# Performance work log

Hardware: AMD Instinct MI355X
Metric: run time of the kernel (lower is better)

Reference implementation:

```python
import jax, jax.numpy as jnp
import numpy as np

DIM = 768
HEADS = 12
HEAD_DIM = DIM // HEADS          # 64
M = int(DIM * 0.5)               # 384 random features
HIDDEN = int(DIM * 4.0)          # 3072
SCALE = HEAD_DIM ** (-0.25)
EPSILON = 1e-8
LN_EPS = 1e-5


def _orf(key):
    # per-head block-orthogonal random features, scaled by sqrt(m)
    def one(k):
        a = jax.random.normal(k, (M, HEAD_DIM))
        q, _ = jnp.linalg.qr(a)          # (M, HEAD_DIM), orthonormal columns
        return q.T                        # (HEAD_DIM, M), orthonormal rows
    ks = jax.random.split(key, HEADS)
    return jax.vmap(one)(ks) * np.sqrt(M)  # (H, HEAD_DIM, M)


def setup_inputs() -> dict:
    key = jax.random.key(0)
    ks = jax.random.split(key, 8)
    s = 0.02
    return {
        "x": jax.random.normal(ks[0], (32, 1024, DIM), jnp.float32),
        "ln1_g": jnp.ones((DIM,), jnp.float32),
        "ln1_b": jnp.zeros((DIM,), jnp.float32),
        "qkv_w": jax.random.normal(ks[1], (DIM, 3 * DIM), jnp.float32) * s,
        "qkv_b": jnp.zeros((3 * DIM,), jnp.float32),
        "w_orf": _orf(ks[2]).astype(jnp.float32),
        "proj_w": jax.random.normal(ks[3], (DIM, DIM), jnp.float32) * s,
        "proj_b": jnp.zeros((DIM,), jnp.float32),
        "ln2_g": jnp.ones((DIM,), jnp.float32),
        "ln2_b": jnp.zeros((DIM,), jnp.float32),
        "fc1_w": jax.random.normal(ks[4], (DIM, HIDDEN), jnp.float32) * s,
        "fc1_b": jnp.zeros((HIDDEN,), jnp.float32),
        "fc2_w": jax.random.normal(ks[5], (HIDDEN, DIM), jnp.float32) * s,
        "fc2_b": jnp.zeros((DIM,), jnp.float32),
    }


def _layernorm(x, g, b):
    mu = jnp.mean(x, axis=-1, keepdims=True)
    var = jnp.mean(jnp.square(x - mu), axis=-1, keepdims=True)
    return (x - mu) * jax.lax.rsqrt(var + LN_EPS) * g + b


def _feature_map(x, w):
    # x: (B,H,N,C), w: (H,C,M) -> exp(x*scale @ w - ||x*scale||^2/2)/sqrt(M)
    xs = x * SCALE
    proj = jnp.einsum("bhnc,hcm->bhnm", xs, w)
    sq = 0.5 * jnp.sum(xs * xs, axis=-1, keepdims=True)
    return jnp.exp(proj - sq) / np.sqrt(M)


def _performer_attn(x, qkv_w, qkv_b, w_orf, proj_w, proj_b):
    B, N, _ = x.shape
    qkv = x @ qkv_w + qkv_b                       # (B,N,3*DIM)
    qkv = qkv.reshape(B, N, 3, HEADS, HEAD_DIM)
    qkv = jnp.transpose(qkv, (2, 0, 3, 1, 4))     # (3,B,H,N,C)
    q = _feature_map(qkv[0], w_orf)               # (B,H,N,M)
    k = _feature_map(qkv[1], w_orf)               # (B,H,N,M)
    v = qkv[2]                                    # (B,H,N,C)
    k_sum = jnp.sum(k, axis=2)                    # (B,H,M)
    D = jnp.einsum("bhnm,bhm->bhn", q, k_sum)[..., None] + EPSILON
    ktv = jnp.einsum("bhnm,bhnc->bhmc", k, v)     # (B,H,M,C)
    out = jnp.einsum("bhnm,bhmc->bhnc", q, ktv) / D
    out = jnp.transpose(out, (0, 2, 1, 3)).reshape(B, N, DIM)
    return out @ proj_w + proj_b


def reference(x, ln1_g, ln1_b, qkv_w, qkv_b, w_orf, proj_w, proj_b,
              ln2_g, ln2_b, fc1_w, fc1_b, fc2_w, fc2_b):
    h = x + _performer_attn(_layernorm(x, ln1_g, ln1_b),
                            qkv_w, qkv_b, w_orf, proj_w, proj_b)
    y = _layernorm(h, ln2_g, ln2_b)
    y = jax.nn.gelu(y @ fc1_w + fc1_b) @ fc2_w + fc2_b
    return h + y
```

## Files before the change

### kernel.cpp

```cpp
#include <hip/hip_runtime.h>
#include <hip/hip_bf16.h>

#define NTOK   32768
#define BATCH  32
#define SEQ    1024
#define DIMD   768
#define HEADS  12
#define HDIM   64
#define MFEAT  384
#define HIDDEN 3072
#define SCALE  0.35355339059327379f
#define HALF_SCALE2 0.0625f
#define EPSP   3.84e-6f
#define WSCL   64.0f
#define IWSCL  0.015625f

typedef __attribute__((ext_vector_type(8))) short bf16x8;
typedef __attribute__((ext_vector_type(4))) float f32x4;
typedef __attribute__((ext_vector_type(2))) long long llong2;

static __device__ __forceinline__ float bf2f(unsigned short u) {
    return __uint_as_float(((unsigned)u) << 16);
}
static __device__ __forceinline__ unsigned short f2bf(float f) {
    unsigned u = __float_as_uint(f);
    return (unsigned short)((u + 0x7FFFu + ((u >> 16) & 1u)) >> 16);
}
static __device__ __forceinline__ unsigned char f2e4m3(float f) {
    unsigned u = __float_as_uint(f);
    const unsigned char s = (unsigned char)((u >> 24) & 0x80);
    const float af = __uint_as_float(u & 0x7FFFFFFF);
    if (!(af < 464.0f)) return s | 0x7E;
    int e = (int)((u >> 23) & 0xFF) - 127;
    if (e < -6) e = -6;
    const float ulp = __uint_as_float((unsigned)((e - 3 + 127) << 23));
    const float q = rintf(af / ulp) * ulp;
    if (q == 0.0f) return s;
    const unsigned v = __float_as_uint(q);
    const int qe = (int)((v >> 23) & 0xFF) - 127;
    if (qe < -6) return s | (unsigned char)(q * 512.0f);
    return s | (unsigned char)(((qe + 7) << 3) | ((v >> 20) & 7));
}
static __device__ __forceinline__ unsigned char f2e4m3_hw(float v) {
    unsigned r = 0;
    asm("v_cvt_pk_fp8_f32 %0, %1, %1" : "+v"(r) : "v"(v));
    return (unsigned char)(r & 0xFF);
}
static __device__ __forceinline__ int kperm(int kl) {
    return ((kl & 31) >> 3) * 16 + ((kl >> 5) << 3) + (kl & 7);
}
static __device__ __forceinline__ float gelu_fast(float v) {
    const float c = 0.7978845608028654f;
    const float u = c * v * (1.0f + 0.044715f * v * v);
    return v / (1.0f + __expf(-2.0f * u));
}
static __device__ __forceinline__ void gload16(const void* g, void* l) {
    __builtin_amdgcn_global_load_lds(
        (const __attribute__((address_space(1))) void*)g,
        (__attribute__((address_space(3))) void*)l, 16, 0, 0);
}

template <int OT>
__global__ __launch_bounds__(256) void ln_vec(
    const float* __restrict__ x, const float* __restrict__ g,
    const float* __restrict__ bta, void* __restrict__ o) {
    const size_t row = blockIdx.x;
    const float* xr = x + row * DIMD;
    const int t = threadIdx.x;
    float4 v = make_float4(0.f, 0.f, 0.f, 0.f);
    if (t < 192) v = *(const float4*)(xr + t * 4);
    float s  = v.x + v.y + v.z + v.w;
    float sq = v.x * v.x + v.y * v.y + v.z * v.z + v.w * v.w;
    const int lane = t & 63, w = t >> 6;
    #pragma unroll
    for (int off = 32; off > 0; off >>= 1) {
        s  += __shfl_down(s, off, 64);
        sq += __shfl_down(sq, off, 64);
    }
    __shared__ float red[2][4];
    if (lane == 0) { red[0][w] = s; red[1][w] = sq; }
    __syncthreads();
    s  = red[0][0] + red[0][1] + red[0][2] + red[0][3];
    sq = red[1][0] + red[1][1] + red[1][2] + red[1][3];
    const float mu  = s * (1.0f / DIMD);
    const float var = sq * (1.0f / DIMD) - mu * mu;
    const float r = rsqrtf(var + 1e-5f);
    if (t < 192) {
        const float4 gv = *(const float4*)(g + t * 4);
        const float4 bv = *(const float4*)(bta + t * 4);
        const float o0 = (v.x - mu) * r * gv.x + bv.x;
        const float o1 = (v.y - mu) * r * gv.y + bv.y;
        const float o2 = (v.z - mu) * r * gv.z + bv.z;
        const float o3 = (v.w - mu) * r * gv.w + bv.w;
        if constexpr (OT == 1) {
            unsigned short* orow = (unsigned short*)o + row * DIMD + t * 4;
            *(ushort4*)orow = make_ushort4(f2bf(o0), f2bf(o1), f2bf(o2), f2bf(o3));
        } else {
            const int k = t * 4;
            const int kb = k & ~63, kl = k & 63;
            unsigned char* orow = (unsigned char*)o + row * DIMD + kb + kperm(kl);
            uchar4 p; p.x = f2e4m3(o0); p.y = f2e4m3(o1);
            p.z = f2e4m3(o2); p.w = f2e4m3(o3);
            *(uchar4*)orow = p;
        }
    }
}

__global__ __launch_bounds__(256) void wconv(
    const float* __restrict__ W, unsigned short* __restrict__ Wt, int K, int N) {
    __shared__ float tile[32][33];
    const int n0 = blockIdx.x << 5, k0 = blockIdx.y << 5;
    const int tn = threadIdx.x & 31, tg = threadIdx.x >> 5;
    #pragma unroll
    for (int i = 0; i < 4; ++i) {
        const int k = (tg << 2) + i;
        tile[k][tn] = W[(size_t)(k0 + k) * N + n0 + tn];
    }
    __syncthreads();
    #pragma unroll
    for (int i = 0; i < 4; ++i) {
        const int n = (tg << 2) + i;
        Wt[(size_t)(n0 + n) * K + k0 + tn] = f2bf(tile[tn][n]);
    }
}

__global__ __launch_bounds__(256) void wconv_f8(
    const float* __restrict__ W, unsigned char* __restrict__ Wt, int K, int N) {
    __shared__ float tile[32][33];
    const int n0 = blockIdx.x << 5, k0 = blockIdx.y << 5;
    const int tn = threadIdx.x & 31, tg = threadIdx.x >> 5;
    #pragma unroll
    for (int i = 0; i < 4; ++i) {
        const int k = (tg << 2) + i;
        tile[k][tn] = W[(size_t)(k0 + k) * N + n0 + tn];
    }
    __syncthreads();
    #pragma unroll
    for (int i = 0; i < 4; ++i) {
        const int n = (tg << 2) + i;
        const int k = k0 + tn;
        const int kb = k & ~63, kl = k & 63;
        Wt[(size_t)(n0 + n) * K + kb + kperm(kl)] = f2e4m3(WSCL * tile[tn][n]);
    }
}

__global__ __launch_bounds__(256) void wprep(
    const float* __restrict__ worf, unsigned short* __restrict__ worf_ts) {
    __shared__ float tile[32][33];
    const int m0 = blockIdx.x << 5, c0 = blockIdx.y << 5, h = blockIdx.z;
    const int tn = threadIdx.x & 31, tg = threadIdx.x >> 5;
    #pragma unroll
    for (int i = 0; i < 4; ++i) {
        const int c = (tg << 2) + i;
        tile[c][tn] = worf[(size_t)(h * HDIM + c0 + c) * MFEAT + m0 + tn];
    }
    __syncthreads();
    #pragma unroll
    for (int i = 0; i < 4; ++i) {
        const int m = (tg << 2) + i;
        worf_ts[(size_t)(h * MFEAT + m0 + m) * HDIM + c0 + tn] =
            f2bf(SCALE * tile[tn][m]);
    }
}

template <int ACT, bool RES, bool OBF16>
__global__ __launch_bounds__(256, 2) void gemm_mfma(
    const unsigned short* __restrict__ A, const unsigned short* __restrict__ Wt,
    const float* __restrict__ bias, const float* __restrict__ resid,
    void* __restrict__ Craw, int K, int N) {
    __shared__ unsigned short As[3][128 * 32];
    __shared__ unsigned short Bs[3][128 * 32];
    const int t = threadIdx.x;
    const int w = t >> 6, l = t & 63;
    const int ncol = gridDim.x;
    const int lin = blockIdx.y * ncol + blockIdx.x;
    const int cpx = (ncol * gridDim.y) >> 3;
    const int wg = (lin & 7) * cpx + (lin >> 3);
    const int row0 = (wg / ncol) << 7, col0 = (wg % ncol) << 7;
    const int wr = (w >> 1) << 6, wc = (w & 1) << 6;

    const int sc = (((l & 3) ^ ((l >> 3) & 3)) << 3);
    const unsigned short* ag0 = A  + (size_t)(row0 + w * 32 + (l >> 2)) * K + sc;
    const unsigned short* ag1 = ag0 + (size_t)16 * K;
    const unsigned short* bg0 = Wt + (size_t)(col0 + w * 32 + (l >> 2)) * K + sc;
    const unsigned short* bg1 = bg0 + (size_t)16 * K;

    f32x4 acc[4][4] = {};
    const int NT = K >> 5;

    auto stage = [&](int bi, int s) {
        const size_t ko = (size_t)s << 5;
        gload16(ag0 + ko, &As[bi][w * 1024]);
        gload16(ag1 + ko, &As[bi][w * 1024 + 512]);
        gload16(bg0 + ko, &Bs[bi][w * 1024]);
        gload16(bg1 + ko, &Bs[bi][w * 1024 + 512]);
    };

    stage(0, 0);
    stage(1, 1);
    const int lr = l & 15, lg = l >> 4;
    const int lkx = (lg << 3) ^ ((((lr >> 1) & 3)) << 3);
    int cur = 0;
    for (int s = 0; s < NT; ++s) {
        if (s + 1 < NT) asm volatile("s_waitcnt vmcnt(4)" ::: "memory");
        else            asm volatile("s_waitcnt vmcnt(0)" ::: "memory");
        __builtin_amdgcn_s_barrier();
        __builtin_amdgcn_sched_barrier(0);
        if (s + 2 < NT) {
            int sb = cur + 2; if (sb >= 3) sb -= 3;
            stage(sb, s + 2);
        }
        const unsigned short* ab = &As[cur][0];
        const unsigned short* bb = &Bs[cur][0];
        bf16x8 af[4], bfr[4];
        #pragma unroll
        for (int f = 0; f < 4; ++f) {
            af[f]  = *(const bf16x8*)(ab + (wr + f * 16 + lr) * 32 + lkx);
            bfr[f] = *(const bf16x8*)(bb + (wc + f * 16 + lr) * 32 + lkx);
        }
        #pragma unroll
        for (int fi = 0; fi < 4; ++fi)
            #pragma unroll
            for (int fj = 0; fj < 4; ++fj)
                acc[fi][fj] = __builtin_amdgcn_mfma_f32_16x16x32_bf16(
                    af[fi], bfr[fj], acc[fi][fj], 0, 0, 0);
        cur = (cur + 1 == 3) ? 0 : cur + 1;
    }

    float bv[4];
    #pragma unroll
    for (int fj = 0; fj < 4; ++fj) bv[fj] = bias[col0 + wc + fj * 16 + lr];
    #pragma unroll
    for (int fi = 0; fi < 4; ++fi) {
        #pragma unroll
        for (int r = 0; r < 4; ++r) {
            const int row = row0 + wr + fi * 16 + lg * 4 + r;
            const size_t base = (size_t)row * N + col0 + wc + lr;
            #pragma unroll
            for (int fj = 0; fj < 4; ++fj) {
                float v = acc[fi][fj][r] + bv[fj];
                if constexpr (RES) v += resid[base + fj * 16];
                if constexpr (ACT == 1) v = gelu_fast(v);
                if constexpr (OBF16) ((unsigned short*)Craw)[base + fj * 16] = f2bf(v);
                else                 ((float*)Craw)[base + fj * 16] = v;
            }
        }
    }
}

template <int ACT, bool RES, int OT>
__global__ __launch_bounds__(256, 2) void gemm_fp8(
    const unsigned char* __restrict__ A, const unsigned char* __restrict__ Wt,
    const float* __restrict__ bias, const float* __restrict__ resid,
    void* __restrict__ Craw, int K, int N) {
    __shared__ unsigned char As[3][8192];
    __shared__ unsigned char Bs[3][8192];
    const int t = threadIdx.x;
    const int w = t >> 6, l = t & 63;
    const int ncol = gridDim.x;
    const int lin = blockIdx.y * ncol + blockIdx.x;
    const int cpx = (ncol * gridDim.y) >> 3;
    const int wg = (lin & 7) * cpx + (lin >> 3);
    const int row0 = (wg / ncol) << 7, col0 = (wg % ncol) << 7;
    const int wr = (w >> 1) << 6, wc = (w & 1) << 6;

    const int sc = (((l & 3) ^ ((l >> 3) & 3)) << 4);
    const unsigned char* ag0 = A  + (size_t)(row0 + w * 32 + (l >> 2)) * K + sc;
    const unsigned char* ag1 = ag0 + (size_t)16 * K;
    const unsigned char* bg0 = Wt + (size_t)(col0 + w * 32 + (l >> 2)) * K + sc;
    const unsigned char* bg1 = bg0 + (size_t)16 * K;

    f32x4 acc[4][4] = {};
    const int NT = K >> 6;

    auto stage = [&](int bi, int s) {
        const size_t ko = (size_t)s << 6;
        gload16(ag0 + ko, &As[bi][w * 2048]);
        gload16(ag1 + ko, &As[bi][w * 2048 + 1024]);
        gload16(bg0 + ko, &Bs[bi][w * 2048]);
        gload16(bg1 + ko, &Bs[bi][w * 2048 + 1024]);
    };

    stage(0, 0);
    stage(1, 1);
    const int lr = l & 15, lg = l >> 4;
    const int xoff = ((lg ^ ((lr >> 1) & 3)) << 4);
    int cur = 0;
    for (int s = 0; s < NT; ++s) {
        if (s + 1 < NT) asm volatile("s_waitcnt vmcnt(4)" ::: "memory");
        else            asm volatile("s_waitcnt vmcnt(0)" ::: "memory");
        __builtin_amdgcn_s_barrier();
        __builtin_amdgcn_sched_barrier(0);
        if (s + 2 < NT) {
            int sb = cur + 2; if (sb >= 3) sb -= 3;
            stage(sb, s + 2);
        }
        const unsigned char* ab = &As[cur][0];
        const unsigned char* bb = &Bs[cur][0];
        llong2 av[4], bvv[4];
        #pragma unroll
        for (int f = 0; f < 4; ++f) {
            av[f]  = *(const llong2*)(ab + ((wr + f * 16 + lr) << 6) + xoff);
            bvv[f] = *(const llong2*)(bb + ((wc + f * 16 + lr) << 6) + xoff);
        }
        #pragma unroll
        for (int ks = 0; ks < 2; ++ks)
            #pragma unroll
            for (int fi = 0; fi < 4; ++fi)
                #pragma unroll
                for (int fj = 0; fj < 4; ++fj)
                    acc[fi][fj] = __builtin_amdgcn_mfma_f32_16x16x32_fp8_fp8(
                        av[fi][ks], bvv[fj][ks], acc[fi][fj], 0, 0, 0);
        cur = (cur + 1 == 3) ? 0 : cur + 1;
    }

    float bv[4];
    #pragma unroll
    for (int fj = 0; fj < 4; ++fj) bv[fj] = bias[col0 + wc + fj * 16 + lr];
    #pragma unroll
    for (int fi = 0; fi < 4; ++fi) {
        #pragma unroll
        for (int r = 0; r < 4; ++r) {
            const int row = row0 + wr + fi * 16 + lg * 4 + r;
            const size_t base = (size_t)row * N + col0 + wc + lr;
            #pragma unroll
            for (int fj = 0; fj < 4; ++fj) {
                float v = acc[fi][fj][r] * IWSCL + bv[fj];
                if constexpr (RES) v += resid[base + fj * 16];
                if constexpr (ACT == 1) v = gelu_fast(v);
                if constexpr (OT == 2) {
                    const int cl = (fj << 4) + lr;
                    ((unsigned char*)Craw)[(size_t)row * N + col0 + wc + kperm(cl)] =
                        f2e4m3_hw(v);
                } else {
                    ((float*)Craw)[base + fj * 16] = v;
                }
            }
        }
    }
}

__global__ __launch_bounds__(256, 1) void ktv_mfma(
    const unsigned short* __restrict__ qkvb,
    const unsigned short* __restrict__ worf_ts,
    unsigned short* __restrict__ ktvT) {
    const int h = blockIdx.x, b = blockIdx.y, bh = b * HEADS + h;
    __shared__ __align__(16) unsigned short Klds[32][72];
    __shared__ __align__(16) unsigned short VT[80][40];
    __shared__ __align__(16) unsigned short P[4][96][40];
    const int t = threadIdx.x, w = t >> 6, l = t & 63;
    const int lr = l & 15, lg = l >> 4;
    const int m0 = w * 96;

    bf16x8 bfw[6][2];
    #pragma unroll
    for (int mt = 0; mt < 6; ++mt)
        #pragma unroll
        for (int ks = 0; ks < 2; ++ks)
            bfw[mt][ks] = *(const bf16x8*)(worf_ts +
                (size_t)(h * MFEAT + m0 + mt * 16 + lr) * HDIM + ks * 32 + lg * 8);

    f32x4 acc[5][6] = {};

    for (int i = t; i < 16 * 40; i += 256) {
        const int r = 64 + i / 40, cc = i % 40;
        VT[r][cc] = (r == 64) ? (unsigned short)0x3F80 : (unsigned short)0;
    }
    const unsigned short* kglob = qkvb + (size_t)b * SEQ * 2304 + 768 + h * 64;
    const unsigned short* vglob = kglob + 768;

    for (int n0 = 0; n0 < SEQ; n0 += 32) {
        __syncthreads();
        {
            const int row = t >> 3, c8 = (t & 7) << 3;
            *(bf16x8*)&Klds[row][c8] =
                *(const bf16x8*)(kglob + (size_t)(n0 + row) * 2304 + c8);
        }
        {
            const int n = t & 31, c0 = (t >> 5) << 3;
            const unsigned short* src = vglob + (size_t)(n0 + n) * 2304 + c0;
            ushort4 v0 = *(const ushort4*)src;
            ushort4 v1 = *(const ushort4*)(src + 4);
            VT[c0 + 0][n] = v0.x; VT[c0 + 1][n] = v0.y;
            VT[c0 + 2][n] = v0.z; VT[c0 + 3][n] = v0.w;
            VT[c0 + 4][n] = v1.x; VT[c0 + 5][n] = v1.y;
            VT[c0 + 6][n] = v1.z; VT[c0 + 7][n] = v1.w;
        }
        __syncthreads();

        bf16x8 afk[2][2];
        float sqv[2][4];
        #pragma unroll
        for (int ns = 0; ns < 2; ++ns) {
            float s = 0.f;
            #pragma unroll
            for (int ks = 0; ks < 2; ++ks) {
                afk[ns][ks] = *(const bf16x8*)&Klds[ns * 16 + lr][ks * 32 + lg * 8];
                #pragma unroll
                for (int j = 0; j < 8; ++j) {
                    const float f = bf2f((unsigned short)afk[ns][ks][j]);
                    s += f * f;
                }
            }
            s += __shfl_xor(s, 16);
            s += __shfl_xor(s, 32);
            s *= HALF_SCALE2;
            #pragma unroll
            for (int r = 0; r < 4; ++r)
                sqv[ns][r] = __shfl(s, (lg << 2) + r);
        }

        #pragma unroll
        for (int mt = 0; mt < 6; ++mt) {
            #pragma unroll
            for (int ns = 0; ns < 2; ++ns) {
                f32x4 p = {};
                p = __builtin_amdgcn_mfma_f32_16x16x32_bf16(afk[ns][0], bfw[mt][0], p, 0, 0, 0);
                p = __builtin_amdgcn_mfma_f32_16x16x32_bf16(afk[ns][1], bfw[mt][1], p, 0, 0, 0);
                ushort4 pk;
                pk.x = f2bf(__expf(p[0] - sqv[ns][0]));
                pk.y = f2bf(__expf(p[1] - sqv[ns][1]));
                pk.z = f2bf(__expf(p[2] - sqv[ns][2]));
                pk.w = f2bf(__expf(p[3] - sqv[ns][3]));
                *(ushort4*)&P[w][mt * 16 + lr][ns * 16 + lg * 4] = pk;
            }
        }
        asm volatile("s_waitcnt lgkmcnt(0)" ::: "memory");
        __builtin_amdgcn_sched_barrier(0);

        bf16x8 afv[5];
        #pragma unroll
        for (int ct = 0; ct < 5; ++ct)
            afv[ct] = *(const bf16x8*)&VT[ct * 16 + lr][lg * 8];
        #pragma unroll
        for (int mt = 0; mt < 6; ++mt) {
            const bf16x8 bp = *(const bf16x8*)&P[w][mt * 16 + lr][lg * 8];
            #pragma unroll
            for (int ct = 0; ct < 5; ++ct)
                acc[ct][mt] = __builtin_amdgcn_mfma_f32_16x16x32_bf16(afv[ct], bp, acc[ct][mt], 0, 0, 0);
        }
    }

    unsigned short* dst = ktvT + (size_t)bh * 80 * MFEAT;
    #pragma unroll
    for (int ct = 0; ct < 5; ++ct)
        #pragma unroll
        for (int mt = 0; mt < 6; ++mt)
            #pragma unroll
            for (int r = 0; r < 4; ++r) {
                const int cc = ct * 16 + lg * 4 + r;
                const int m = m0 + mt * 16 + lr;
                dst[(size_t)cc * MFEAT + m] = f2bf(acc[ct][mt][r]);
            }
}

__global__ __launch_bounds__(256) void attn_out_mfma(
    const unsigned short* __restrict__ qkvb,
    const unsigned short* __restrict__ worf_ts,
    const unsigned short* __restrict__ ktvT,
    unsigned short* __restrict__ attn) {
    const int n0 = blockIdx.x << 7;
    const int h = blockIdx.y, b = blockIdx.z, bh = b * HEADS + h;
    __shared__ __align__(16) unsigned short KT[80][104];
    __shared__ __align__(16) unsigned short P[4][32][104];
    const int t = threadIdx.x, w = t >> 6, l = t & 63;
    const int lr = l & 15, lg = l >> 4;
    const int nw = n0 + w * 32;

    bf16x8 bq[2][2];
    float sqn[2];
    #pragma unroll
    for (int nt = 0; nt < 2; ++nt) {
        float s = 0.f;
        #pragma unroll
        for (int ks = 0; ks < 2; ++ks) {
            bq[nt][ks] = *(const bf16x8*)(qkvb +
                (size_t)(b * SEQ + nw + nt * 16 + lr) * 2304 + h * 64 + ks * 32 + lg * 8);
            #pragma unroll
            for (int j = 0; j < 8; ++j) {
                const float f = bf2f((unsigned short)bq[nt][ks][j]);
                s += f * f;
            }
        }
        s += __shfl_xor(s, 16);
        s += __shfl_xor(s, 32);
        sqn[nt] = s * HALF_SCALE2;
    }

    f32x4 acc[5][2] = {};
    const unsigned short* ktg = ktvT + (size_t)bh * 80 * MFEAT;

    for (int ch = 0; ch < 4; ++ch) {
        const int m0 = ch * 96;
        __syncthreads();
        for (int i = t; i < 1920; i += 256) {
            const int row = i / 24, q = i % 24;
            *(ushort4*)&KT[row][q * 4] =
                *(const ushort4*)(ktg + (size_t)row * MFEAT + m0 + q * 4);
        }
        __syncthreads();

        #pragma unroll
        for (int mt = 0; mt < 6; ++mt) {
            bf16x8 afw[2];
            #pragma unroll
            for (int ks = 0; ks < 2; ++ks)
                afw[ks] = *(const bf16x8*)(worf_ts +
                    (size_t)(h * MFEAT + m0 + mt * 16 + lr) * HDIM + ks * 32 + lg * 8);
            #pragma unroll
            for (int nt = 0; nt < 2; ++nt) {
                f32x4 p = {};
                p = __builtin_amdgcn_mfma_f32_16x16x32_bf16(afw[0], bq[nt][0], p, 0, 0, 0);
                p = __builtin_amdgcn_mfma_f32_16x16x32_bf16(afw[1], bq[nt][1], p, 0, 0, 0);
                ushort4 pk;
                pk.x = f2bf(__expf(p[0] - sqn[nt]));
                pk.y = f2bf(__expf(p[1] - sqn[nt]));
                pk.z = f2bf(__expf(p[2] - sqn[nt]));
                pk.w = f2bf(__expf(p[3] - sqn[nt]));
                *(ushort4*)&P[w][nt * 16 + lr][mt * 16 + lg * 4] = pk;
            }
        }
        asm volatile("s_waitcnt lgkmcnt(0)" ::: "memory");
        __builtin_amdgcn_sched_barrier(0);

        #pragma unroll
        for (int ks = 0; ks < 3; ++ks) {
            bf16x8 bp[2];
            #pragma unroll
            for (int nt = 0; nt < 2; ++nt)
                bp[nt] = *(const bf16x8*)&P[w][nt * 16 + lr][ks * 32 + lg * 8];
            #pragma unroll
            for (int ct = 0; ct < 5; ++ct) {
                const bf16x8 av = *(const bf16x8*)&KT[ct * 16 + lr][ks * 32 + lg * 8];
                #pragma unroll
                for (int nt = 0; nt < 2; ++nt)
                    acc[ct][nt] = __builtin_amdgcn_mfma_f32_16x16x32_bf16(av, bp[nt], acc[ct][nt], 0, 0, 0);
            }
        }
    }

    #pragma unroll
    for (int nt = 0; nt < 2; ++nt) {
        const float d = __shfl(acc[4][nt][0], lr);
        const float inv = 1.0f / (d + EPSP);
        const int token = b * SEQ + nw + nt * 16 + lr;
        #pragma unroll
        for (int ct = 0; ct < 4; ++ct)
            #pragma unroll
            for (int r = 0; r < 4; ++r) {
                const int cc = ct * 16 + lg * 4 + r;
                attn[(size_t)token * DIMD + h * 64 + cc] = f2bf(acc[ct][nt][r] * inv);
            }
    }
}

extern "C" void kernel_launch(void* const* d_in, const int* in_sizes, int n_in,
                              void* d_out, int out_size, void* d_ws, size_t ws_size,
                              hipStream_t stream) {
    const float* x      = (const float*)d_in[0];
    const float* ln1_g  = (const float*)d_in[1];
    const float* ln1_b  = (const float*)d_in[2];
    const float* qkv_w  = (const float*)d_in[3];
    const float* qkv_b  = (const float*)d_in[4];
    const float* w_orf  = (const float*)d_in[5];
    const float* proj_w = (const float*)d_in[6];
    const float* proj_b = (const float*)d_in[7];
    const float* ln2_g  = (const float*)d_in[8];
    const float* ln2_b  = (const float*)d_in[9];
    const float* fc1_w  = (const float*)d_in[10];
    const float* fc1_b  = (const float*)d_in[11];
    const float* fc2_w  = (const float*)d_in[12];
    const float* fc2_b  = (const float*)d_in[13];
    float* out = (float*)d_out;

    char* wsb = (char*)d_ws;
    unsigned short* qkvb    = (unsigned short*)wsb;
    unsigned short* attn    = (unsigned short*)(wsb + 150994944);
    unsigned short* ktvT    = (unsigned short*)(wsb + 201326592);
    unsigned short* worf_ts = (unsigned short*)(wsb + 224919552);
    unsigned char*  y2f8    = (unsigned char*)(wsb + 201326592);
    unsigned char*  hidf8   = (unsigned char*)wsb;
    unsigned short* qkv_wt  = (unsigned short*)(wsb + 251658240);
    unsigned short* proj_wt = (unsigned short*)(wsb + 255197184);
    unsigned char*  fc1_wf8 = (unsigned char*)(wsb + 256376832);
    unsigned char*  fc2_wf8 = (unsigned char*)(wsb + 261095424);
    unsigned short* xln     = (unsigned short*)d_out;

    wconv<<<dim3(2304 / 32, 768 / 32), 256, 0, stream>>>(qkv_w, qkv_wt, DIMD, 2304);
    wconv<<<dim3(768 / 32, 768 / 32), 256, 0, stream>>>(proj_w, proj_wt, DIMD, DIMD);
    wconv_f8<<<dim3(3072 / 32, 768 / 32), 256, 0, stream>>>(fc1_w, fc1_wf8, DIMD, HIDDEN);
    wconv_f8<<<dim3(768 / 32, 3072 / 32), 256, 0, stream>>>(fc2_w, fc2_wf8, HIDDEN, DIMD);
    wprep<<<dim3(MFEAT / 32, HDIM / 32, HEADS), 256, 0, stream>>>(w_orf, worf_ts);
    ln_vec<1><<<NTOK, 256, 0, stream>>>(x, ln1_g, ln1_b, xln);
    gemm_mfma<0, false, true><<<dim3(2304 / 128, NTOK / 128), 256, 0, stream>>>(
        xln, qkv_wt, qkv_b, nullptr, qkvb, DIMD, 2304);
    ktv_mfma<<<dim3(HEADS, BATCH), 256, 0, stream>>>(qkvb, worf_ts, ktvT);
    attn_out_mfma<<<dim3(SEQ / 128, HEADS, BATCH), 256, 0, stream>>>(
        qkvb, worf_ts, ktvT, attn);
    gemm_mfma<0, true, false><<<dim3(DIMD / 128, NTOK / 128), 256, 0, stream>>>(
        attn, proj_wt, proj_b, x, out, DIMD, DIMD);
    ln_vec<2><<<NTOK, 256, 0, stream>>>(out, ln2_g, ln2_b, y2f8);
    gemm_fp8<1, false, 2><<<dim3(HIDDEN / 128, NTOK / 128), 256, 0, stream>>>(
        y2f8, fc1_wf8, fc1_b, nullptr, hidf8, DIMD, HIDDEN);
    gemm_fp8<0, true, 0><<<dim3(DIMD / 128, NTOK / 128), 256, 0, stream>>>(
        hidf8, fc2_wf8, fc2_b, out, out, HIDDEN, DIMD);
}
```

Baseline: 793.4 us.

## Use BK=64 double-buffered LDS pipeline with 8-way XOR swizzle in MFMA GEMM

Changes the GEMM main loop from a 3-stage pipeline with a K-tile of 32 to a 2-stage pipeline with a K-tile of 64, using a wider 8-way XOR swizzle for LDS. This halves the number of barriers and loop iterations per K and doubles the MFMA work between synchronisations. The trade-off is shallower prefetch (one stage ahead with a full vmcnt(0) wait) and the same 64KB of LDS, so latency hiding may get worse.

```diff
diff --git a/kernel.cpp b/kernel.cpp
--- a/kernel.cpp
+++ b/kernel.cpp
@@ -168,8 +168,8 @@
     const unsigned short* __restrict__ A, const unsigned short* __restrict__ Wt,
     const float* __restrict__ bias, const float* __restrict__ resid,
     void* __restrict__ Craw, int K, int N) {
-    __shared__ unsigned short As[3][128 * 32];
-    __shared__ unsigned short Bs[3][128 * 32];
+    __shared__ unsigned short As[2][128 * 64];
+    __shared__ unsigned short Bs[2][128 * 64];
     const int t = threadIdx.x;
     const int w = t >> 6, l = t & 63;
     const int ncol = gridDim.x;
@@ -179,52 +179,57 @@
     const int row0 = (wg / ncol) << 7, col0 = (wg % ncol) << 7;
     const int wr = (w >> 1) << 6, wc = (w & 1) << 6;
 
-    const int sc = (((l & 3) ^ ((l >> 3) & 3)) << 3);
-    const unsigned short* ag0 = A  + (size_t)(row0 + w * 32 + (l >> 2)) * K + sc;
-    const unsigned short* ag1 = ag0 + (size_t)16 * K;
-    const unsigned short* bg0 = Wt + (size_t)(col0 + w * 32 + (l >> 2)) * K + sc;
-    const unsigned short* bg1 = bg0 + (size_t)16 * K;
+    const int swz = (((l & 7) ^ ((l >> 3) & 7)) << 3);
+    const unsigned short* ag[4];
+    const unsigned short* bg[4];
+    #pragma unroll
+    for (int j = 0; j < 4; ++j) {
+        const int r = w * 32 + j * 8 + (l >> 3);
+        ag[j] = A  + (size_t)(row0 + r) * K + swz;
+        bg[j] = Wt + (size_t)(col0 + r) * K + swz;
+    }
 
     f32x4 acc[4][4] = {};
-    const int NT = K >> 5;
+    const int NT = K >> 6;
 
     auto stage = [&](int bi, int s) {
-        const size_t ko = (size_t)s << 5;
-        gload16(ag0 + ko, &As[bi][w * 1024]);
-        gload16(ag1 + ko, &As[bi][w * 1024 + 512]);
-        gload16(bg0 + ko, &Bs[bi][w * 1024]);
-        gload16(bg1 + ko, &Bs[bi][w * 1024 + 512]);
+        const size_t ko = (size_t)s << 6;
+        #pragma unroll
+        for (int j = 0; j < 4; ++j)
+            gload16(ag[j] + ko, &As[bi][(w * 32 + j * 8) * 64]);
+        #pragma unroll
+        for (int j = 0; j < 4; ++j)
+            gload16(bg[j] + ko, &Bs[bi][(w * 32 + j * 8) * 64]);
     };
 
     stage(0, 0);
-    stage(1, 1);
     const int lr = l & 15, lg = l >> 4;
-    const int lkx = (lg << 3) ^ ((((lr >> 1) & 3)) << 3);
-    int cur = 0;
+    const int c0 = ((lg ^ (lr & 7)) << 3);
     for (int s = 0; s < NT; ++s) {
-        if (s + 1 < NT) asm volatile("s_waitcnt vmcnt(4)" ::: "memory");
-        else            asm volatile("s_waitcnt vmcnt(0)" ::: "memory");
+        asm volatile("s_waitcnt vmcnt(0)" ::: "memory");
         __builtin_amdgcn_s_barrier();
         __builtin_amdgcn_sched_barrier(0);
-        if (s + 2 < NT) {
-            int sb = cur + 2; if (sb >= 3) sb -= 3;
-            stage(sb, s + 2);
-        }
-        const unsigned short* ab = &As[cur][0];
-        const unsigned short* bb = &Bs[cur][0];
-        bf16x8 af[4], bfr[4];
+        if (s + 1 < NT) stage((s + 1) & 1, s + 1);
+        const unsigned short* ab = &As[s & 1][0];
+        const unsigned short* bb = &Bs[s & 1][0];
+        bf16x8 af[4][2], bfr[4][2];
         #pragma unroll
         for (int f = 0; f < 4; ++f) {
-            af[f]  = *(const bf16x8*)(ab + (wr + f * 16 + lr) * 32 + lkx);
-            bfr[f] = *(const bf16x8*)(bb + (wc + f * 16 + lr) * 32 + lkx);
-        }
-        #pragma unroll
-        for (int fi = 0; fi < 4; ++fi)
-            #pragma unroll
-            for (int fj = 0; fj < 4; ++fj)
-                acc[fi][fj] = __builtin_amdgcn_mfma_f32_16x16x32_bf16(
-                    af[fi], bfr[fj], acc[fi][fj], 0, 0, 0);
-        cur = (cur + 1 == 3) ? 0 : cur + 1;
+            const int ra = (wr + f * 16 + lr) << 6;
+            const int rb = (wc + f * 16 + lr) << 6;
+            af[f][0]  = *(const bf16x8*)(ab + ra + c0);
+            af[f][1]  = *(const bf16x8*)(ab + ra + (c0 ^ 32));
+            bfr[f][0] = *(const bf16x8*)(bb + rb + c0);
+            bfr[f][1] = *(const bf16x8*)(bb + rb + (c0 ^ 32));
+        }
+        #pragma unroll
+        for (int ks = 0; ks < 2; ++ks)
+            #pragma unroll
+            for (int fi = 0; fi < 4; ++fi)
+                #pragma unroll
+                for (int fj = 0; fj < 4; ++fj)
+                    acc[fi][fj] = __builtin_amdgcn_mfma_f32_16x16x32_bf16(
+                        af[fi][ks], bfr[fj][ks], acc[fi][fj], 0, 0, 0);
     }
 
     float bv[4];
```

New measurement: 795.9 us. No clear change (+0.3%).

## Switch FP8 MLP GEMMs to scaled 16x16x128 MX MFMA with 128-wide K tiles

Applied to the files above, without the earlier changes.

Replaces the fp8 16x16x32 MFMA inner loop with the gfx950 scaled MFMA (16x16x128 f8f6f4). The weight scale is folded into the hardware block scale instead of an epilogue multiply. K tiles grow to 128 with a matching 128-element permutation in the LN, weight-conversion and fc1 output layouts. Pipelining drops from a 3-stage buffer with partial vmcnt waits to a double buffer that waits for all loads, which may expose more load latency. GELU division becomes a fast reciprocal.

```diff
diff --git a/kernel.cpp b/kernel.cpp
--- a/kernel.cpp
+++ b/kernel.cpp
@@ -13,11 +13,13 @@
 #define HALF_SCALE2 0.0625f
 #define EPSP   3.84e-6f
 #define WSCL   64.0f
-#define IWSCL  0.015625f
+#define SCA_ONE   0x7F7F7F7Fu
+#define SCB_I64   0x79797979u
 
 typedef __attribute__((ext_vector_type(8))) short bf16x8;
 typedef __attribute__((ext_vector_type(4))) float f32x4;
 typedef __attribute__((ext_vector_type(2))) long long llong2;
+typedef __attribute__((ext_vector_type(8))) int i32x8;
 
 static __device__ __forceinline__ float bf2f(unsigned short u) {
     return __uint_as_float(((unsigned)u) << 16);
@@ -46,13 +48,13 @@
     asm("v_cvt_pk_fp8_f32 %0, %1, %1" : "+v"(r) : "v"(v));
     return (unsigned char)(r & 0xFF);
 }
-static __device__ __forceinline__ int kperm(int kl) {
-    return ((kl & 31) >> 3) * 16 + ((kl >> 5) << 3) + (kl & 7);
+static __device__ __forceinline__ int kp128(int kl) {
+    return (((kl >> 4) & 1) << 6) + ((kl >> 5) << 4) + (kl & 15);
 }
 static __device__ __forceinline__ float gelu_fast(float v) {
     const float c = 0.7978845608028654f;
     const float u = c * v * (1.0f + 0.044715f * v * v);
-    return v / (1.0f + __expf(-2.0f * u));
+    return v * __builtin_amdgcn_rcpf(1.0f + __expf(-2.0f * u));
 }
 static __device__ __forceinline__ void gload16(const void* g, void* l) {
     __builtin_amdgcn_global_load_lds(
@@ -97,8 +99,8 @@
             *(ushort4*)orow = make_ushort4(f2bf(o0), f2bf(o1), f2bf(o2), f2bf(o3));
         } else {
             const int k = t * 4;
-            const int kb = k & ~63, kl = k & 63;
-            unsigned char* orow = (unsigned char*)o + row * DIMD + kb + kperm(kl);
+            const int gb = k & ~127, kl = k & 127;
+            unsigned char* orow = (unsigned char*)o + row * DIMD + gb + kp128(kl);
             uchar4 p; p.x = f2e4m3(o0); p.y = f2e4m3(o1);
             p.z = f2e4m3(o2); p.w = f2e4m3(o3);
             *(uchar4*)orow = p;
@@ -139,8 +141,8 @@
     for (int i = 0; i < 4; ++i) {
         const int n = (tg << 2) + i;
         const int k = k0 + tn;
-        const int kb = k & ~63, kl = k & 63;
-        Wt[(size_t)(n0 + n) * K + kb + kperm(kl)] = f2e4m3(WSCL * tile[tn][n]);
+        const int gb = k & ~127, kl = k & 127;
+        Wt[(size_t)(n0 + n) * K + gb + kp128(kl)] = f2e4m3(WSCL * tile[tn][n]);
     }
 }
 
@@ -249,12 +251,12 @@
 }
 
 template <int ACT, bool RES, int OT>
-__global__ __launch_bounds__(256, 2) void gemm_fp8(
+__global__ __launch_bounds__(256, 2) void gemm_mx(
     const unsigned char* __restrict__ A, const unsigned char* __restrict__ Wt,
     const float* __restrict__ bias, const float* __restrict__ resid,
     void* __restrict__ Craw, int K, int N) {
-    __shared__ unsigned char As[3][8192];
-    __shared__ unsigned char Bs[3][8192];
+    __shared__ unsigned char As0[2][8192], As1[2][8192];
+    __shared__ unsigned char Bs0[2][8192], Bs1[2][8192];
     const int t = threadIdx.x;
     const int w = t >> 6, l = t & 63;
     const int ncol = gridDim.x;
@@ -265,53 +267,55 @@
     const int wr = (w >> 1) << 6, wc = (w & 1) << 6;
 
     const int sc = (((l & 3) ^ ((l >> 3) & 3)) << 4);
-    const unsigned char* ag0 = A  + (size_t)(row0 + w * 32 + (l >> 2)) * K + sc;
-    const unsigned char* ag1 = ag0 + (size_t)16 * K;
-    const unsigned char* bg0 = Wt + (size_t)(col0 + w * 32 + (l >> 2)) * K + sc;
-    const unsigned char* bg1 = bg0 + (size_t)16 * K;
+    const size_t arow0 = (size_t)(row0 + w * 32 + (l >> 2)) * K;
+    const size_t arow1 = arow0 + (size_t)16 * K;
+    const size_t brow0 = (size_t)(col0 + w * 32 + (l >> 2)) * K;
+    const size_t brow1 = brow0 + (size_t)16 * K;
 
     f32x4 acc[4][4] = {};
-    const int NT = K >> 6;
+    const int NT = K >> 7;
 
     auto stage = [&](int bi, int s) {
-        const size_t ko = (size_t)s << 6;
-        gload16(ag0 + ko, &As[bi][w * 2048]);
-        gload16(ag1 + ko, &As[bi][w * 2048 + 1024]);
-        gload16(bg0 + ko, &Bs[bi][w * 2048]);
-        gload16(bg1 + ko, &Bs[bi][w * 2048 + 1024]);
+        const size_t ko = (size_t)s << 7;
+        gload16(A + arow0 + ko + sc,      &As0[bi][w * 2048]);
+        gload16(A + arow1 + ko + sc,      &As0[bi][w * 2048 + 1024]);
+        gload16(A + arow0 + ko + 64 + sc, &As1[bi][w * 2048]);
+        gload16(A + arow1 + ko + 64 + sc, &As1[bi][w * 2048 + 1024]);
+        gload16(Wt + brow0 + ko + sc,      &Bs0[bi][w * 2048]);
+        gload16(Wt + brow1 + ko + sc,      &Bs0[bi][w * 2048 + 1024]);
+        gload16(Wt + brow0 + ko + 64 + sc, &Bs1[bi][w * 2048]);
+        gload16(Wt + brow1 + ko + 64 + sc, &Bs1[bi][w * 2048 + 1024]);
     };
 
     stage(0, 0);
-    stage(1, 1);
     const int lr = l & 15, lg = l >> 4;
     const int xoff = ((lg ^ ((lr >> 1) & 3)) << 4);
-    int cur = 0;
     for (int s = 0; s < NT; ++s) {
-        if (s + 1 < NT) asm volatile("s_waitcnt vmcnt(4)" ::: "memory");
-        else            asm volatile("s_waitcnt vmcnt(0)" ::: "memory");
+        asm volatile("s_waitcnt vmcnt(0)" ::: "memory");
         __builtin_amdgcn_s_barrier();
         __builtin_amdgcn_sched_barrier(0);
-        if (s + 2 < NT) {
-            int sb = cur + 2; if (sb >= 3) sb -= 3;
-            stage(sb, s + 2);
-        }
-        const unsigned char* ab = &As[cur][0];
-        const unsigned char* bb = &Bs[cur][0];
-        llong2 av[4], bvv[4];
+        if (s + 1 < NT) stage((s + 1) & 1, s + 1);
+        const unsigned char* a0 = &As0[s & 1][0];
+        const unsigned char* a1 = &As1[s & 1][0];
+        const unsigned char* b0 = &Bs0[s & 1][0];
+        const unsigned char* b1 = &Bs1[s & 1][0];
+        i32x8 afm[4], bfm[4];
         #pragma unroll
         for (int f = 0; f < 4; ++f) {
-            av[f]  = *(const llong2*)(ab + ((wr + f * 16 + lr) << 6) + xoff);
-            bvv[f] = *(const llong2*)(bb + ((wc + f * 16 + lr) << 6) + xoff);
-        }
-        #pragma unroll
-        for (int ks = 0; ks < 2; ++ks)
-            #pragma unroll
-            for (int fi = 0; fi < 4; ++fi)
-                #pragma unroll
-                for (int fj = 0; fj < 4; ++fj)
-                    acc[fi][fj] = __builtin_amdgcn_mfma_f32_16x16x32_fp8_fp8(
-                        av[fi][ks], bvv[fj][ks], acc[fi][fj], 0, 0, 0);
-        cur = (cur + 1 == 3) ? 0 : cur + 1;
+            const int ra = ((wr + f * 16 + lr) << 6) + xoff;
+            const int rb = ((wc + f * 16 + lr) << 6) + xoff;
+            ((llong2*)&afm[f])[0] = *(const llong2*)(a0 + ra);
+            ((llong2*)&afm[f])[1] = *(const llong2*)(a1 + ra);
+            ((llong2*)&bfm[f])[0] = *(const llong2*)(b0 + rb);
+            ((llong2*)&bfm[f])[1] = *(const llong2*)(b1 + rb);
+        }
+        #pragma unroll
+        for (int fi = 0; fi < 4; ++fi)
+            #pragma unroll
+            for (int fj = 0; fj < 4; ++fj)
+                acc[fi][fj] = __builtin_amdgcn_mfma_scale_f32_16x16x128_f8f6f4(
+                    afm[fi], bfm[fj], acc[fi][fj], 0, 0,
+                    0, SCA_ONE, 0, SCB_I64);
     }
 
     float bv[4];
@@ -325,12 +329,12 @@
             const size_t base = (size_t)row * N + col0 + wc + lr;
             #pragma unroll
             for (int fj = 0; fj < 4; ++fj) {
-                float v = acc[fi][fj][r] * IWSCL + bv[fj];
+                float v = acc[fi][fj][r] + bv[fj];
                 if constexpr (RES) v += resid[base + fj * 16];
                 if constexpr (ACT == 1) v = gelu_fast(v);
                 if constexpr (OT == 2) {
-                    const int cl = (fj << 4) + lr;
-                    ((unsigned char*)Craw)[(size_t)row * N + col0 + wc + kperm(cl)] =
+                    const int cl = wc + fj * 16 + lr;
+                    ((unsigned char*)Craw)[(size_t)row * N + col0 + kp128(cl)] =
                         f2e4m3_hw(v);
                 } else {
                     ((float*)Craw)[base + fj * 16] = v;
@@ -600,8 +604,8 @@
     gemm_mfma<0, true, false><<<dim3(DIMD / 128, NTOK / 128), 256, 0, stream>>>(
         attn, proj_wt, proj_b, x, out, DIMD, DIMD);
     ln_vec<2><<<NTOK, 256, 0, stream>>>(out, ln2_g, ln2_b, y2f8);
-    gemm_fp8<1, false, 2><<<dim3(HIDDEN / 128, NTOK / 128), 256, 0, stream>>>(
+    gemm_mx<1, false, 2><<<dim3(HIDDEN / 128, NTOK / 128), 256, 0, stream>>>(
         y2f8, fc1_wf8, fc1_b, nullptr, hidf8, DIMD, HIDDEN);
-    gemm_fp8<0, true, 0><<<dim3(DIMD / 128, NTOK / 128), 256, 0, stream>>>(
+    gemm_mx<0, true, 0><<<dim3(DIMD / 128, NTOK / 128), 256, 0, stream>>>(
         hidf8, fc2_wf8, fc2_b, out, out, HIDDEN, DIMD);
 }
```

Measured after the change: 748.7 us. 5.6% less time.
